# Optimization experiments

Measured on AMD Instinct MI355X. Metric: run time of the kernel, lower is better.

Reference implementation:

```python
import jax, jax.numpy as jnp
import numpy as np

D_MODEL = 256
NCODES = 32


def setup_inputs() -> dict:
    key = jax.random.key(0)
    k1, k2 = jax.random.split(key)
    B, L = 64, 2048
    rev_repr = jax.random.normal(k1, (B, L, D_MODEL), dtype=jnp.float32)
    # xavier_normal for Linear(256 -> ncodes): std = sqrt(2/(fan_in+fan_out))
    std = (2.0 / (D_MODEL + NCODES)) ** 0.5
    W_codes = jax.random.normal(k2, (NCODES, D_MODEL), dtype=jnp.float32) * std
    return {"rev_repr": rev_repr, "W_codes": W_codes}


def reference(rev_repr, W_codes):
    # scores: (B, L, ncodes) = rev_repr @ W_codes.T
    scores = jnp.einsum('bld,kd->blk', rev_repr, W_codes)
    # softmax over the L (sequence) dimension, dim=1
    wts = jax.nn.softmax(scores, axis=1)
    # fused weighted-sum pooling: (B, ncodes, 256) — avoids (B,L,ncodes,256) intermediate
    contexts = jnp.einsum('blk,bld->bkd', wts, rev_repr)
    return contexts
```

## Files before the change

### kernel.cpp

```cpp
#include <hip/hip_runtime.h>
#include <math.h>

#define BATCH 64
#define LSEQ 2048
#define DMOD 256
#define KC 32
#define LCHUNK 256
#define LS 32
#define NSUB 8
#define PITCH_D 264
#define PITCH_L 40

typedef __bf16 bf16x8 __attribute__((ext_vector_type(8)));
typedef __bf16 bf16x4 __attribute__((ext_vector_type(4)));
typedef float f32x4 __attribute__((ext_vector_type(4)));

__global__ __launch_bounds__(256, 2) void fused_pool_kernel(
    const float* __restrict__ rev, const float* __restrict__ W,
    float* __restrict__ cPartial, float* __restrict__ zPartial) {
  __shared__ __align__(16) __bf16 sW[KC * PITCH_D];
  __shared__ __align__(16) __bf16 sRev[LS * PITCH_D];
  __shared__ __align__(16) __bf16 sRevT[DMOD * PITCH_L];
  __shared__ __align__(16) __bf16 sP[KC * PITCH_L];
  __shared__ float sZw[2][KC];

  const int tid = threadIdx.x;
  const int b = blockIdx.y;
  const int lc = blockIdx.x;
  const int lbase = lc * LCHUNK;
  const int wave = tid >> 6;
  const int lane = tid & 63;
  const int col = lane & 15;
  const int quad = lane >> 4;

  const int Mt = wave & 1;
  const int Nt = wave >> 1;

#pragma unroll
  for (int i = 0; i < 8; ++i) {
    int flat = tid + 256 * i;
    int kk = flat >> 6, c4 = flat & 63;
    float4 v = *(const float4*)(W + kk * DMOD + c4 * 4);
    bf16x4 h = {(__bf16)v.x, (__bf16)v.y, (__bf16)v.z, (__bf16)v.w};
    *(bf16x4*)(&sW[kk * PITCH_D + c4 * 4]) = h;
  }

  f32x4 acc2[8];
#pragma unroll
  for (int i = 0; i < 8; ++i) acc2[i] = (f32x4){0.f, 0.f, 0.f, 0.f};
  float zacc[4] = {0.f, 0.f, 0.f, 0.f};

  for (int sub = 0; sub < NSUB; ++sub) {
    const int l0 = lbase + sub * LS;
    __syncthreads();
#pragma unroll
    for (int i = 0; i < 8; ++i) {
      int slot = tid + 256 * i;
      int r = slot >> 6, c4 = slot & 63;
      float4 v = *(const float4*)(rev + ((size_t)b * LSEQ + l0 + r) * DMOD + c4 * 4);
      bf16x4 h = {(__bf16)v.x, (__bf16)v.y, (__bf16)v.z, (__bf16)v.w};
      *(bf16x4*)(&sRev[r * PITCH_D + c4 * 4]) = h;
    }
    __syncthreads();

#pragma unroll
    for (int j4 = 0; j4 < 4; ++j4) {
      bf16x8 v;
#pragma unroll
      for (int j = 0; j < 8; ++j) v[j] = sRev[(j4 * 8 + j) * PITCH_D + tid];
      *(bf16x8*)(&sRevT[tid * PITCH_L + j4 * 8]) = v;
    }

    f32x4 acc1 = {0.f, 0.f, 0.f, 0.f};
#pragma unroll
    for (int ks = 0; ks < 8; ++ks) {
      bf16x8 afrag = *(const bf16x8*)(&sW[(Mt * 16 + col) * PITCH_D + ks * 32 + quad * 8]);
      bf16x8 bfrag = *(const bf16x8*)(&sRev[(Nt * 16 + col) * PITCH_D + ks * 32 + quad * 8]);
      acc1 = __builtin_amdgcn_mfma_f32_16x16x32_bf16(afrag, bfrag, acc1, 0, 0, 0);
    }
#pragma unroll
    for (int reg = 0; reg < 4; ++reg) {
      float p = __expf(acc1[reg]);
      __bf16 ph = (__bf16)p;
      zacc[reg] += (float)ph;
      sP[(Mt * 16 + quad * 4 + reg) * PITCH_L + Nt * 16 + col] = ph;
    }
    __syncthreads();

    bf16x8 pa = *(const bf16x8*)(&sP[(Mt * 16 + col) * PITCH_L + quad * 8]);
#pragma unroll
    for (int nt = 0; nt < 8; ++nt) {
      int dt = Nt * 8 + nt;
      bf16x8 bb = *(const bf16x8*)(&sRevT[(dt * 16 + col) * PITCH_L + quad * 8]);
      acc2[nt] = __builtin_amdgcn_mfma_f32_16x16x32_bf16(pa, bb, acc2[nt], 0, 0, 0);
    }
  }

#pragma unroll
  for (int off = 1; off < 16; off <<= 1)
#pragma unroll
    for (int reg = 0; reg < 4; ++reg) zacc[reg] += __shfl_xor(zacc[reg], off, 64);
  if (col == 0) {
#pragma unroll
    for (int reg = 0; reg < 4; ++reg)
      sZw[Nt][Mt * 16 + quad * 4 + reg] = zacc[reg];
  }
  __syncthreads();
  if (tid < KC)
    zPartial[((size_t)b * 8 + lc) * KC + tid] = sZw[0][tid] + sZw[1][tid];

  float* dst = cPartial + (((size_t)b * 8 + lc) * KC) * DMOD;
#pragma unroll
  for (int nt = 0; nt < 8; ++nt) {
    int d = (Nt * 8 + nt) * 16 + col;
#pragma unroll
    for (int reg = 0; reg < 4; ++reg) {
      int k = Mt * 16 + quad * 4 + reg;
      dst[k * DMOD + d] = acc2[nt][reg];
    }
  }
}

__global__ __launch_bounds__(256) void reduce_kernel(
    const float* __restrict__ cPartial, const float* __restrict__ zPartial,
    float* __restrict__ out) {
  int idx = blockIdx.x * 256 + threadIdx.x;
  int b = idx >> 13;
  int k = (idx >> 8) & 31;
  int d = idx & 255;
  float s = 0.f, z = 0.f;
#pragma unroll
  for (int lcc = 0; lcc < 8; ++lcc) {
    s += cPartial[(((size_t)b * 8 + lcc) * KC + k) * DMOD + d];
    z += zPartial[((size_t)b * 8 + lcc) * KC + k];
  }
  out[idx] = s / z;
}

extern "C" void kernel_launch(void* const* d_in, const int* in_sizes, int n_in,
                              void* d_out, int out_size, void* d_ws,
                              size_t ws_size, hipStream_t stream) {
  const float* rev = (const float*)d_in[0];
  const float* W = (const float*)d_in[1];
  float* out = (float*)d_out;

  float* ws = (float*)d_ws;
  float* cPartial = ws;
  float* zPartial = cPartial + (size_t)BATCH * 8 * KC * DMOD;

  fused_pool_kernel<<<dim3(8, BATCH), dim3(256), 0, stream>>>(rev, W, cPartial,
                                                              zPartial);
  reduce_kernel<<<dim3(2048), dim3(256), 0, stream>>>(cPartial, zPartial, out);
}
```

Measured before the change: 196.6 us.

## Halve L chunk per block, keep W fragments in registers, raise occupancy

Splits each batch's sequence into 16 chunks of 128 instead of 8 of 256, doubling the grid to 1024 blocks for better CU coverage. W is loaded directly into per-wave register fragments instead of being staged in shared memory, which frees LDS and allows launch bounds of 4 blocks per CU. The sRev pitch also changes from 264 to 260. In exchange, the partial-context buffer and the reduce kernel's work double, since it now sums 16 partials per output, and the new pitch may change LDS bank conflicts.

```diff
diff --git a/kernel.cpp b/kernel.cpp
--- a/kernel.cpp
+++ b/kernel.cpp
@@ -5,20 +5,20 @@
 #define LSEQ 2048
 #define DMOD 256
 #define KC 32
-#define LCHUNK 256
+#define LCHUNK 128
+#define NCHUNK 16
 #define LS 32
-#define NSUB 8
-#define PITCH_D 264
+#define NSUB 4
+#define PITCH_D 260
 #define PITCH_L 40
 
 typedef __bf16 bf16x8 __attribute__((ext_vector_type(8)));
 typedef __bf16 bf16x4 __attribute__((ext_vector_type(4)));
 typedef float f32x4 __attribute__((ext_vector_type(4)));
 
-__global__ __launch_bounds__(256, 2) void fused_pool_kernel(
+__global__ __launch_bounds__(256, 4) void fused_pool_kernel(
     const float* __restrict__ rev, const float* __restrict__ W,
     float* __restrict__ cPartial, float* __restrict__ zPartial) {
-  __shared__ __align__(16) __bf16 sW[KC * PITCH_D];
   __shared__ __align__(16) __bf16 sRev[LS * PITCH_D];
   __shared__ __align__(16) __bf16 sRevT[DMOD * PITCH_L];
   __shared__ __align__(16) __bf16 sP[KC * PITCH_L];
@@ -36,13 +36,16 @@
   const int Mt = wave & 1;
   const int Nt = wave >> 1;
 
+  bf16x8 wfrag[8];
+  {
+    const float* wp = W + (Mt * 16 + col) * DMOD + quad * 8;
 #pragma unroll
-  for (int i = 0; i < 8; ++i) {
-    int flat = tid + 256 * i;
-    int kk = flat >> 6, c4 = flat & 63;
-    float4 v = *(const float4*)(W + kk * DMOD + c4 * 4);
-    bf16x4 h = {(__bf16)v.x, (__bf16)v.y, (__bf16)v.z, (__bf16)v.w};
-    *(bf16x4*)(&sW[kk * PITCH_D + c4 * 4]) = h;
+    for (int ks = 0; ks < 8; ++ks) {
+      float4 va = *(const float4*)(wp + ks * 32);
+      float4 vb = *(const float4*)(wp + ks * 32 + 4);
+      wfrag[ks] = (bf16x8){(__bf16)va.x, (__bf16)va.y, (__bf16)va.z, (__bf16)va.w,
+                           (__bf16)vb.x, (__bf16)vb.y, (__bf16)vb.z, (__bf16)vb.w};
+    }
   }
 
   f32x4 acc2[8];
@@ -74,9 +77,8 @@
     f32x4 acc1 = {0.f, 0.f, 0.f, 0.f};
 #pragma unroll
     for (int ks = 0; ks < 8; ++ks) {
-      bf16x8 afrag = *(const bf16x8*)(&sW[(Mt * 16 + col) * PITCH_D + ks * 32 + quad * 8]);
       bf16x8 bfrag = *(const bf16x8*)(&sRev[(Nt * 16 + col) * PITCH_D + ks * 32 + quad * 8]);
-      acc1 = __builtin_amdgcn_mfma_f32_16x16x32_bf16(afrag, bfrag, acc1, 0, 0, 0);
+      acc1 = __builtin_amdgcn_mfma_f32_16x16x32_bf16(wfrag[ks], bfrag, acc1, 0, 0, 0);
     }
 #pragma unroll
     for (int reg = 0; reg < 4; ++reg) {
@@ -107,9 +109,9 @@
   }
   __syncthreads();
   if (tid < KC)
-    zPartial[((size_t)b * 8 + lc) * KC + tid] = sZw[0][tid] + sZw[1][tid];
+    zPartial[((size_t)b * NCHUNK + lc) * KC + tid] = sZw[0][tid] + sZw[1][tid];
 
-  float* dst = cPartial + (((size_t)b * 8 + lc) * KC) * DMOD;
+  float* dst = cPartial + (((size_t)b * NCHUNK + lc) * KC) * DMOD;
 #pragma unroll
   for (int nt = 0; nt < 8; ++nt) {
     int d = (Nt * 8 + nt) * 16 + col;
@@ -130,9 +132,9 @@
   int d = idx & 255;
   float s = 0.f, z = 0.f;
 #pragma unroll
-  for (int lcc = 0; lcc < 8; ++lcc) {
-    s += cPartial[(((size_t)b * 8 + lcc) * KC + k) * DMOD + d];
-    z += zPartial[((size_t)b * 8 + lcc) * KC + k];
+  for (int lcc = 0; lcc < NCHUNK; ++lcc) {
+    s += cPartial[(((size_t)b * NCHUNK + lcc) * KC + k) * DMOD + d];
+    z += zPartial[((size_t)b * NCHUNK + lcc) * KC + k];
   }
   out[idx] = s / z;
 }
@@ -146,9 +148,9 @@
 
   float* ws = (float*)d_ws;
   float* cPartial = ws;
-  float* zPartial = cPartial + (size_t)BATCH * 8 * KC * DMOD;
+  float* zPartial = cPartial + (size_t)BATCH * NCHUNK * KC * DMOD;
 
-  fused_pool_kernel<<<dim3(8, BATCH), dim3(256), 0, stream>>>(rev, W, cPartial,
-                                                              zPartial);
+  fused_pool_kernel<<<dim3(NCHUNK, BATCH), dim3(256), 0, stream>>>(rev, W, cPartial,
+                                                                   zPartial);
   reduce_kernel<<<dim3(2048), dim3(256), 0, stream>>>(cPartial, zPartial, out);
 }
```

New measurement: 206.7 us. +5.1%, slower.
